# Optimization experiments

Hardware: AMD Instinct MI355X
Metric: run time of the kernel (lower is better)

Reference implementation:

```python
import jax, jax.numpy as jnp
import numpy as np

B, D, C = 512, 512, 100000
M1, M2, M3 = 1.0, 0.5, 0.0  # canonical ArcFace margins
EPS = 1e-12  # tf.nn.l2_normalize epsilon


def _l2norm(v, axis):
    return v * jax.lax.rsqrt(jnp.maximum(jnp.sum(v * v, axis=axis, keepdims=True), EPS))


def setup_inputs() -> dict:
    key = jax.random.key(0)
    k1, k2, k3 = jax.random.split(key, 3)
    x = jax.random.normal(k1, (B, D), dtype=jnp.float32)
    W = jax.random.normal(k2, (D, C), dtype=jnp.float32)
    label_idx = jax.random.randint(k3, (B,), 0, C, dtype=jnp.int32)
    return {"x": x, "W": W, "label_idx": label_idx}


def reference(x, W, label_idx):
    xn = _l2norm(x, axis=1)            # [B, D] unit embeddings
    Wn = _l2norm(W, axis=0)            # [D, C] unit class weights (norm=True fc)
    logits = xn @ Wn                   # [B, C] cosine similarities
    # gather target cosine per row (gather_nd over one-hot label)
    t = jnp.take_along_axis(logits, label_idx[:, None], axis=1)[:, 0]  # [B]
    # m1 == 1.0 -> skip angular scaling branch; m2 != 0 -> additive angular margin
    t = jnp.arccos(t) + M2
    # clamp to pi value-wise, straight-through gradient: t1 = t + pi - stop_grad(t)
    t = jnp.minimum(t, t + (jnp.pi - jax.lax.stop_gradient(t)))
    t = jnp.cos(t)
    onehot = jax.nn.one_hot(label_idx, C, dtype=logits.dtype)  # [B, C]
    out = logits * (1.0 - onehot) + t[:, None] * onehot
    out = out - onehot * M3
    return out
```

## Files before the change

### kernel.cpp

```cpp
#include <hip/hip_runtime.h>
#include <math.h>

#define BB 512
#define DD 512
#define CC 100000
#define MARGIN2 0.5f
#define PI_F 3.14159265358979323846f

#define BM 256
#define BN 128
#define BK 64
#define KSTEPS (DD / BK)
#define NPAN 782
#define GRID (2 * NPAN)

typedef __bf16 bf16x8 __attribute__((ext_vector_type(8)));
typedef float f32x4 __attribute__((ext_vector_type(4)));

static __device__ __forceinline__ unsigned short f2bf(float f) {
    union { float f; unsigned u; } v; v.f = f;
    unsigned r = v.u + 0x7FFFu + ((v.u >> 16) & 1u);
    return (unsigned short)(r >> 16);
}

static __device__ __forceinline__ int swz(int row, int kbyte) {
    return row * 128 + (kbyte ^ ((row & 7) << 4));
}

static __device__ __forceinline__ void gll16(const unsigned char* g, unsigned char* l) {
    __builtin_amdgcn_global_load_lds(
        (const __attribute__((address_space(1))) void*)g,
        (__attribute__((address_space(3))) void*)l, 16, 0, 0);
}

__global__ __launch_bounds__(256) void k_norm_x(const float* __restrict__ x,
                                                unsigned char* __restrict__ img) {
    const int lane = threadIdx.x & 63;
    const int row  = blockIdx.x * 4 + (threadIdx.x >> 6);
    const float* xr = x + (size_t)row * DD;
    float4 v0 = *(const float4*)(xr + lane * 4);
    float4 v1 = *(const float4*)(xr + lane * 4 + 256);
    float s = v0.x*v0.x + v0.y*v0.y + v0.z*v0.z + v0.w*v0.w
            + v1.x*v1.x + v1.y*v1.y + v1.z*v1.z + v1.w*v1.w;
    #pragma unroll
    for (int m = 32; m; m >>= 1) s += __shfl_xor(s, m, 64);
    float rs = rsqrtf(fmaxf(s, 1e-12f));
    ushort4 o0, o1;
    o0.x = f2bf(v0.x * rs); o0.y = f2bf(v0.y * rs);
    o0.z = f2bf(v0.z * rs); o0.w = f2bf(v0.w * rs);
    o1.x = f2bf(v1.x * rs); o1.y = f2bf(v1.y * rs);
    o1.z = f2bf(v1.z * rs); o1.w = f2bf(v1.w * rs);

    const int mb   = row >> 8;
    const int lrow = row & 255;
    const int k0   = lane * 4;
    const int t0   = k0 >> 6;
    const int c8   = (k0 >> 3) & 7;
    const int sub  = (k0 >> 2) & 1;
    const int base = (mb * 8 + t0) * 32768 + lrow * 128
                   + ((c8 * 16) ^ ((lrow & 7) << 4)) + sub * 8;
    *(ushort4*)(img + base)          = o0;
    *(ushort4*)(img + base + 131072) = o1;
}

#define LDSZ (65536 + 32768 + 512)

__global__ __launch_bounds__(512, 2) void k_gemm(const unsigned char* __restrict__ img,
                                                 const float* __restrict__ W,
                                                 float* __restrict__ out) {
    __shared__ __align__(16) unsigned char LDS[LDSZ];
    unsigned char* bufA = LDS;
    unsigned char* bufB = LDS + 65536;
    float* rn = (float*)(LDS + 98304);

    const int tid = threadIdx.x;
    const int bid = blockIdx.x;

    const int xcd = bid & 7;
    const int jj  = bid >> 3;
    const int v   = (xcd < 4) ? (xcd * 196 + jj) : (784 + (xcd - 4) * 195 + jj);
    const int mb  = v & 1;
    const int nb  = v >> 1;
    const int M0 = mb * BM;
    const int N0 = nb * BN;

    const int lane = tid & 63;
    const int wid  = tid >> 6;
    const int wm = wid >> 1;
    const int wn = wid & 1;
    const int lr = lane & 15;
    const int lg = lane >> 4;

    int b_go[4], b_ld[4];
    #pragma unroll
    for (int i = 0; i < 4; ++i) {
        int s  = tid + i * 512;
        int n  = s & 127;
        int kq = s >> 7;
        int col = N0 + n;
        col = col < CC ? col : CC - 1;
        b_go[i] = kq * 4 * CC + col;
        b_ld[i] = n * 128 + ((kq * 8) ^ ((n & 7) << 4));
    }

    const unsigned char* imgA = img + mb * (8 * 32768);
    const int lds_u = wid * 1024;

    float bregA[4][4], bregB[4][4];
    float bsq[4] = {0.f, 0.f, 0.f, 0.f};

#define LOAD_B(BREG, T) do {                                                   \
    _Pragma("unroll")                                                          \
    for (int i = 0; i < 4; ++i) {                                              \
        const float* p = W + b_go[i] + (T) * (BK * CC);                        \
        BREG[i][0] = p[0];      BREG[i][1] = p[CC];                            \
        BREG[i][2] = p[2 * CC]; BREG[i][3] = p[3 * CC];                        \
    } } while (0)

#define GLL_A(T) do {                                                          \
    unsigned char* A_nxt = bufA + ((T) & 1) * 32768;                           \
    const unsigned char* gsrc = imgA + (T) * 32768;                            \
    _Pragma("unroll")                                                          \
    for (int i = 0; i < 4; ++i)                                                \
        gll16(gsrc + i * 8192 + lds_u + lane * 16, A_nxt + i * 8192 + lds_u);  \
    } while (0)

#define WRITE_B(BREG, T) do {                                                  \
    unsigned char* dst = bufB + ((T) & 1) * 16384;                             \
    _Pragma("unroll")                                                          \
    for (int i = 0; i < 4; ++i) {                                              \
        bsq[i] += BREG[i][0] * BREG[i][0] + BREG[i][1] * BREG[i][1]            \
                + BREG[i][2] * BREG[i][2] + BREG[i][3] * BREG[i][3];           \
        unsigned w0, w1;                                                       \
        asm("v_cvt_pk_bf16_f32 %0, %1, %2" : "=v"(w0) : "v"(BREG[i][0]), "v"(BREG[i][1])); \
        asm("v_cvt_pk_bf16_f32 %0, %1, %2" : "=v"(w1) : "v"(BREG[i][2]), "v"(BREG[i][3])); \
        uint2 w; w.x = w0; w.y = w1;                                           \
        *(uint2*)(dst + b_ld[i]) = w;                                          \
    } } while (0)

#define COMPUTE(T) do {                                                        \
    const unsigned char* A_cur = bufA + ((T) & 1) * 32768;                     \
    const unsigned char* B_cur = bufB + ((T) & 1) * 16384;                     \
    _Pragma("unroll")                                                          \
    for (int ks = 0; ks < 2; ++ks) {                                           \
        bf16x8 af[4], bfr[4];                                                  \
        _Pragma("unroll")                                                      \
        for (int mf = 0; mf < 4; ++mf)                                         \
            af[mf] = *(const bf16x8*)(A_cur + swz(wm * 64 + mf * 16 + lr, ks * 64 + lg * 16)); \
        _Pragma("unroll")                                                      \
        for (int nf = 0; nf < 4; ++nf)                                         \
            bfr[nf] = *(const bf16x8*)(B_cur + swz(wn * 64 + nf * 16 + lr, ks * 64 + lg * 16)); \
        _Pragma("unroll")                                                      \
        for (int mf = 0; mf < 4; ++mf)                                         \
            _Pragma("unroll")                                                  \
            for (int nf = 0; nf < 4; ++nf)                                     \
                acc[mf][nf] = __builtin_amdgcn_mfma_f32_16x16x32_bf16(         \
                    bfr[nf], af[mf], acc[mf][nf], 0, 0, 0);                    \
    } } while (0)

#define KBODY(T, BC, BN_) do {                                                 \
    if ((T) + 1 < KSTEPS) GLL_A((T) + 1);            \
    if ((T) + 2 < KSTEPS) LOAD_B(BN_, (T) + 2);                                \
    __builtin_amdgcn_sched_barrier(0);                                         \
    COMPUTE(T);                                                                \
    if ((T) + 1 < KSTEPS) {                                                    \
        WRITE_B(BC, (T) + 1);                                                  \
        if ((T) + 2 < KSTEPS) { asm volatile("s_waitcnt vmcnt(16)" ::: "memory"); } \
        else                  { asm volatile("s_waitcnt vmcnt(0)"  ::: "memory"); } \
        __builtin_amdgcn_sched_barrier(0);                                     \
        asm volatile("s_waitcnt lgkmcnt(0)" ::: "memory");                     \
        __builtin_amdgcn_sched_barrier(0);                                     \
        __builtin_amdgcn_s_barrier();                                          \
        __builtin_amdgcn_sched_barrier(0);                                     \
    } } while (0)

    f32x4 acc[4][4];
    #pragma unroll
    for (int mf = 0; mf < 4; ++mf)
        #pragma unroll
        for (int nf = 0; nf < 4; ++nf)
            acc[mf][nf] = (f32x4)0.f;

    LOAD_B(bregA, 0);
    GLL_A(0);
    LOAD_B(bregB, 1);
    WRITE_B(bregA, 0);
    asm volatile("s_waitcnt vmcnt(16)" ::: "memory");
    __builtin_amdgcn_sched_barrier(0);
    asm volatile("s_waitcnt lgkmcnt(0)" ::: "memory");
    __builtin_amdgcn_sched_barrier(0);
    __builtin_amdgcn_s_barrier();
    __builtin_amdgcn_sched_barrier(0);

    KBODY(0, bregB, bregA);
    KBODY(1, bregA, bregB);
    KBODY(2, bregB, bregA);
    KBODY(3, bregA, bregB);
    KBODY(4, bregB, bregA);
    KBODY(5, bregA, bregB);
    KBODY(6, bregB, bregA);
    KBODY(7, bregA, bregB);

    __syncthreads();
    float* part = (float*)bufB;
    #pragma unroll
    for (int i = 0; i < 4; ++i)
        part[tid + i * 512] = bsq[i];
    __syncthreads();
    if (tid < BN) {
        float s = 0.f;
        #pragma unroll
        for (int k = 0; k < 16; ++k)
            s += part[k * BN + tid];
        rn[tid] = rsqrtf(fmaxf(s, 1e-12f));
    }
    __syncthreads();

    float* stag = (float*)bufA;
    #pragma unroll
    for (int rd = 0; rd < 8; ++rd) {
        if (wm == (rd >> 1)) {
            #pragma unroll
            for (int f = 0; f < 2; ++f) {
                const int mf = (rd & 1) * 2 + f;
                const int ml = f * 16 + lr;
                #pragma unroll
                for (int nf = 0; nf < 4; ++nf) {
                    const int nl = wn * 64 + nf * 16 + lg * 4;
                    const f32x4 rn4 = *(const f32x4*)(rn + nl);
                    f32x4 o;
                    #pragma unroll
                    for (int r = 0; r < 4; ++r)
                        o[r] = acc[mf][nf][r] * rn4[r];
                    *(f32x4*)(stag + ml * 132 + nl) = o;
                }
            }
        }
        __syncthreads();
        #pragma unroll
        for (int j = tid; j < 1024; j += 512) {
            const int m = j >> 5;
            const int n = (j & 31) * 4;
            if (N0 + n + 4 <= CC) {
                f32x4 o = *(const f32x4*)(stag + m * 132 + n);
                __builtin_nontemporal_store(o,
                    (f32x4*)(out + (size_t)(M0 + rd * 32 + m) * CC + N0 + n));
            }
        }
        __syncthreads();
    }
}

__global__ __launch_bounds__(512) void k_fix(const int* __restrict__ lab,
                                             float* __restrict__ out) {
    const int b = threadIdx.x;
    const int c = lab[b];
    const size_t idx = (size_t)b * CC + c;
    float t = out[idx];
    t = fminf(fmaxf(t, -1.f), 1.f);
    float th = acosf(t) + MARGIN2;
    th = fminf(th, PI_F);
    out[idx] = cosf(th);
}

extern "C" void kernel_launch(void* const* d_in, const int* in_sizes, int n_in,
                              void* d_out, int out_size, void* d_ws, size_t ws_size,
                              hipStream_t stream) {
    const float* x   = (const float*)d_in[0];
    const float* W   = (const float*)d_in[1];
    const int*   lab = (const int*)d_in[2];
    float* out = (float*)d_out;

    unsigned char* img = (unsigned char*)d_ws;

    k_norm_x<<<dim3(BB / 4), dim3(256), 0, stream>>>(x, img);
    k_gemm<<<dim3(GRID), dim3(512), 0, stream>>>(img, W, out);
    k_fix<<<dim3(1), dim3(512), 0, stream>>>(lab, out);
}
```

Baseline: 117.2 us.

## Load A fragments directly from global and shrink LDS for higher occupancy

The normalized x matrix is now written in plain row-major bf16, and each wave loads its MFMA A fragments straight from global memory into registers every k-step. This replaces the pre-swizzled image that was staged through LDS with global_load_lds. LDS use drops to just the double-buffered B tile, and launch bounds go from 2 to 4 blocks per CU so more waves can hide W load latency. The W prefetch is reorganized around a single register buffer: pack and write the next tile, then issue the following load. The trade-offs are unprefetched global A loads on the critical path, which rely on L2 hits, and a tighter VGPR budget that could cause spills.

```diff
diff --git a/kernel.cpp b/kernel.cpp
--- a/kernel.cpp
+++ b/kernel.cpp
@@ -27,14 +27,8 @@
     return row * 128 + (kbyte ^ ((row & 7) << 4));
 }
 
-static __device__ __forceinline__ void gll16(const unsigned char* g, unsigned char* l) {
-    __builtin_amdgcn_global_load_lds(
-        (const __attribute__((address_space(1))) void*)g,
-        (__attribute__((address_space(3))) void*)l, 16, 0, 0);
-}
-
 __global__ __launch_bounds__(256) void k_norm_x(const float* __restrict__ x,
-                                                unsigned char* __restrict__ img) {
+                                                unsigned short* __restrict__ xnb) {
     const int lane = threadIdx.x & 63;
     const int row  = blockIdx.x * 4 + (threadIdx.x >> 6);
     const float* xr = x + (size_t)row * DD;
@@ -50,28 +44,18 @@
     o0.z = f2bf(v0.z * rs); o0.w = f2bf(v0.w * rs);
     o1.x = f2bf(v1.x * rs); o1.y = f2bf(v1.y * rs);
     o1.z = f2bf(v1.z * rs); o1.w = f2bf(v1.w * rs);
-
-    const int mb   = row >> 8;
-    const int lrow = row & 255;
-    const int k0   = lane * 4;
-    const int t0   = k0 >> 6;
-    const int c8   = (k0 >> 3) & 7;
-    const int sub  = (k0 >> 2) & 1;
-    const int base = (mb * 8 + t0) * 32768 + lrow * 128
-                   + ((c8 * 16) ^ ((lrow & 7) << 4)) + sub * 8;
-    *(ushort4*)(img + base)          = o0;
-    *(ushort4*)(img + base + 131072) = o1;
-}
-
-#define LDSZ (65536 + 32768 + 512)
-
-__global__ __launch_bounds__(512, 2) void k_gemm(const unsigned char* __restrict__ img,
+    *(ushort4*)(xnb + (size_t)row * DD + lane * 4)       = o0;
+    *(ushort4*)(xnb + (size_t)row * DD + lane * 4 + 256) = o1;
+}
+
+#define LDSZ (32768 + 512)
+
+__global__ __launch_bounds__(512, 4) void k_gemm(const unsigned short* __restrict__ xnb,
                                                  const float* __restrict__ W,
                                                  float* __restrict__ out) {
     __shared__ __align__(16) unsigned char LDS[LDSZ];
-    unsigned char* bufA = LDS;
-    unsigned char* bufB = LDS + 65536;
-    float* rn = (float*)(LDS + 98304);
+    unsigned char* bufB = LDS;
+    float* rn = (float*)(LDS + 32768);
 
     const int tid = threadIdx.x;
     const int bid = blockIdx.x;
@@ -91,83 +75,82 @@
     const int lr = lane & 15;
     const int lg = lane >> 4;
 
-    int b_go[4], b_ld[4];
-    #pragma unroll
-    for (int i = 0; i < 4; ++i) {
-        int s  = tid + i * 512;
-        int n  = s & 127;
-        int kq = s >> 7;
-        int col = N0 + n;
-        col = col < CC ? col : CC - 1;
-        b_go[i] = kq * 4 * CC + col;
-        b_ld[i] = n * 128 + ((kq * 8) ^ ((n & 7) << 4));
-    }
-
-    const unsigned char* imgA = img + mb * (8 * 32768);
-    const int lds_u = wid * 1024;
-
-    float bregA[4][4], bregB[4][4];
-    float bsq[4] = {0.f, 0.f, 0.f, 0.f};
-
-#define LOAD_B(BREG, T) do {                                                   \
+    const unsigned short* aptr0 = xnb + (size_t)(M0 + wm * 64 +  0 + lr) * DD + lg * 8;
+    const unsigned short* aptr1 = xnb + (size_t)(M0 + wm * 64 + 16 + lr) * DD + lg * 8;
+    const unsigned short* aptr2 = xnb + (size_t)(M0 + wm * 64 + 32 + lr) * DD + lg * 8;
+    const unsigned short* aptr3 = xnb + (size_t)(M0 + wm * 64 + 48 + lr) * DD + lg * 8;
+
+    float    freg[4][4];
+    unsigned pk[8];
+    float    bsq[4] = {0.f, 0.f, 0.f, 0.f};
+    bf16x8   af[8];
+
+#define LOAD_B(T) do {                                                         \
     _Pragma("unroll")                                                          \
     for (int i = 0; i < 4; ++i) {                                              \
-        const float* p = W + b_go[i] + (T) * (BK * CC);                        \
-        BREG[i][0] = p[0];      BREG[i][1] = p[CC];                            \
-        BREG[i][2] = p[2 * CC]; BREG[i][3] = p[3 * CC];                        \
-    } } while (0)
-
-#define GLL_A(T) do {                                                          \
-    unsigned char* A_nxt = bufA + ((T) & 1) * 32768;                           \
-    const unsigned char* gsrc = imgA + (T) * 32768;                            \
-    _Pragma("unroll")                                                          \
-    for (int i = 0; i < 4; ++i)                                                \
-        gll16(gsrc + i * 8192 + lds_u + lane * 16, A_nxt + i * 8192 + lds_u);  \
+        const int s_ = tid + i * 512;                                          \
+        const int n_ = s_ & 127;                                               \
+        const int kq_ = s_ >> 7;                                               \
+        int col_ = N0 + n_; col_ = col_ < CC ? col_ : CC - 1;                  \
+        const float* p = W + (size_t)kq_ * 4 * CC + col_ + (size_t)(T) * (BK * CC); \
+        freg[i][0] = p[0];      freg[i][1] = p[CC];                            \
+        freg[i][2] = p[2 * CC]; freg[i][3] = p[3 * CC];                        \
+    } } while (0)
+
+#define PACK() do {                                                            \
+    _Pragma("unroll")                                                          \
+    for (int i = 0; i < 4; ++i) {                                              \
+        bsq[i] += freg[i][0] * freg[i][0] + freg[i][1] * freg[i][1]            \
+                + freg[i][2] * freg[i][2] + freg[i][3] * freg[i][3];           \
+        asm("v_cvt_pk_bf16_f32 %0, %1, %2" : "=v"(pk[2*i])   : "v"(freg[i][0]), "v"(freg[i][1])); \
+        asm("v_cvt_pk_bf16_f32 %0, %1, %2" : "=v"(pk[2*i+1]) : "v"(freg[i][2]), "v"(freg[i][3])); \
+    } } while (0)
+
+#define WRITE_PK(T) do {                                                       \
+    unsigned char* dst = bufB + ((T) & 1) * 16384;                             \
+    _Pragma("unroll")                                                          \
+    for (int i = 0; i < 4; ++i) {                                              \
+        const int s_ = tid + i * 512;                                          \
+        const int n_ = s_ & 127;                                               \
+        const int kq_ = s_ >> 7;                                               \
+        uint2 w; w.x = pk[2*i]; w.y = pk[2*i+1];                               \
+        *(uint2*)(dst + n_ * 128 + ((kq_ * 8) ^ ((n_ & 7) << 4))) = w;         \
+    } } while (0)
+
+#define LOAD_AF(T) do {                                                        \
+    af[0] = *(const bf16x8*)(aptr0 + (T) * 64);                                \
+    af[1] = *(const bf16x8*)(aptr1 + (T) * 64);                                \
+    af[2] = *(const bf16x8*)(aptr2 + (T) * 64);                                \
+    af[3] = *(const bf16x8*)(aptr3 + (T) * 64);                                \
+    af[4] = *(const bf16x8*)(aptr0 + (T) * 64 + 32);                           \
+    af[5] = *(const bf16x8*)(aptr1 + (T) * 64 + 32);                           \
+    af[6] = *(const bf16x8*)(aptr2 + (T) * 64 + 32);                           \
+    af[7] = *(const bf16x8*)(aptr3 + (T) * 64 + 32);                           \
     } while (0)
 
-#define WRITE_B(BREG, T) do {                                                  \
-    unsigned char* dst = bufB + ((T) & 1) * 16384;                             \
-    _Pragma("unroll")                                                          \
-    for (int i = 0; i < 4; ++i) {                                              \
-        bsq[i] += BREG[i][0] * BREG[i][0] + BREG[i][1] * BREG[i][1]            \
-                + BREG[i][2] * BREG[i][2] + BREG[i][3] * BREG[i][3];           \
-        unsigned w0, w1;                                                       \
-        asm("v_cvt_pk_bf16_f32 %0, %1, %2" : "=v"(w0) : "v"(BREG[i][0]), "v"(BREG[i][1])); \
-        asm("v_cvt_pk_bf16_f32 %0, %1, %2" : "=v"(w1) : "v"(BREG[i][2]), "v"(BREG[i][3])); \
-        uint2 w; w.x = w0; w.y = w1;                                           \
-        *(uint2*)(dst + b_ld[i]) = w;                                          \
-    } } while (0)
-
 #define COMPUTE(T) do {                                                        \
-    const unsigned char* A_cur = bufA + ((T) & 1) * 32768;                     \
     const unsigned char* B_cur = bufB + ((T) & 1) * 16384;                     \
     _Pragma("unroll")                                                          \
     for (int ks = 0; ks < 2; ++ks) {                                           \
-        bf16x8 af[4], bfr[4];                                                  \
         _Pragma("unroll")                                                      \
-        for (int mf = 0; mf < 4; ++mf)                                         \
-            af[mf] = *(const bf16x8*)(A_cur + swz(wm * 64 + mf * 16 + lr, ks * 64 + lg * 16)); \
-        _Pragma("unroll")                                                      \
-        for (int nf = 0; nf < 4; ++nf)                                         \
-            bfr[nf] = *(const bf16x8*)(B_cur + swz(wn * 64 + nf * 16 + lr, ks * 64 + lg * 16)); \
-        _Pragma("unroll")                                                      \
-        for (int mf = 0; mf < 4; ++mf)                                         \
+        for (int nf = 0; nf < 4; ++nf) {                                       \
+            bf16x8 bfr = *(const bf16x8*)(B_cur + swz(wn * 64 + nf * 16 + lr, ks * 64 + lg * 16)); \
             _Pragma("unroll")                                                  \
-            for (int nf = 0; nf < 4; ++nf)                                     \
+            for (int mf = 0; mf < 4; ++mf)                                     \
                 acc[mf][nf] = __builtin_amdgcn_mfma_f32_16x16x32_bf16(         \
-                    bfr[nf], af[mf], acc[mf][nf], 0, 0, 0);                    \
-    } } while (0)
-
-#define KBODY(T, BC, BN_) do {                                                 \
-    if ((T) + 1 < KSTEPS) GLL_A((T) + 1);            \
-    if ((T) + 2 < KSTEPS) LOAD_B(BN_, (T) + 2);                                \
+                    bfr, af[ks * 4 + mf], acc[mf][nf], 0, 0, 0);               \
+        }                                                                      \
+    } } while (0)
+
+#define KBODY(T) do {                                                          \
+    LOAD_AF(T);                                      \
+    __builtin_amdgcn_sched_barrier(0);                                         \
+    if ((T) + 1 < KSTEPS) { PACK(); WRITE_PK((T) + 1); }                       \
+    __builtin_amdgcn_sched_barrier(0);                                         \
+    if ((T) + 2 < KSTEPS) LOAD_B((T) + 2);       \
     __builtin_amdgcn_sched_barrier(0);                                         \
     COMPUTE(T);                                                                \
     if ((T) + 1 < KSTEPS) {                                                    \
-        WRITE_B(BC, (T) + 1);                                                  \
-        if ((T) + 2 < KSTEPS) { asm volatile("s_waitcnt vmcnt(16)" ::: "memory"); } \
-        else                  { asm volatile("s_waitcnt vmcnt(0)"  ::: "memory"); } \
-        __builtin_amdgcn_sched_barrier(0);                                     \
         asm volatile("s_waitcnt lgkmcnt(0)" ::: "memory");                     \
         __builtin_amdgcn_sched_barrier(0);                                     \
         __builtin_amdgcn_s_barrier();                                          \
@@ -181,25 +164,17 @@
         for (int nf = 0; nf < 4; ++nf)
             acc[mf][nf] = (f32x4)0.f;
 
-    LOAD_B(bregA, 0);
-    GLL_A(0);
-    LOAD_B(bregB, 1);
-    WRITE_B(bregA, 0);
-    asm volatile("s_waitcnt vmcnt(16)" ::: "memory");
-    __builtin_amdgcn_sched_barrier(0);
+    LOAD_B(0);
+    PACK();
+    WRITE_PK(0);
+    LOAD_B(1);
     asm volatile("s_waitcnt lgkmcnt(0)" ::: "memory");
     __builtin_amdgcn_sched_barrier(0);
     __builtin_amdgcn_s_barrier();
     __builtin_amdgcn_sched_barrier(0);
 
-    KBODY(0, bregB, bregA);
-    KBODY(1, bregA, bregB);
-    KBODY(2, bregB, bregA);
-    KBODY(3, bregA, bregB);
-    KBODY(4, bregB, bregA);
-    KBODY(5, bregA, bregB);
-    KBODY(6, bregB, bregA);
-    KBODY(7, bregA, bregB);
+    KBODY(0); KBODY(1); KBODY(2); KBODY(3);
+    KBODY(4); KBODY(5); KBODY(6); KBODY(7);
 
     __syncthreads();
     float* part = (float*)bufB;
@@ -216,7 +191,7 @@
     }
     __syncthreads();
 
-    float* stag = (float*)bufA;
+    float* stag = (float*)bufB;
     #pragma unroll
     for (int rd = 0; rd < 8; ++rd) {
         if (wm == (rd >> 1)) {
@@ -271,9 +246,9 @@
     const int*   lab = (const int*)d_in[2];
     float* out = (float*)d_out;
 
-    unsigned char* img = (unsigned char*)d_ws;
-
-    k_norm_x<<<dim3(BB / 4), dim3(256), 0, stream>>>(x, img);
-    k_gemm<<<dim3(GRID), dim3(512), 0, stream>>>(img, W, out);
+    unsigned short* xnb = (unsigned short*)d_ws;
+
+    k_norm_x<<<dim3(BB / 4), dim3(256), 0, stream>>>(x, xnb);
+    k_gemm<<<dim3(GRID), dim3(512), 0, stream>>>(xnb, W, out);
     k_fix<<<dim3(1), dim3(512), 0, stream>>>(lab, out);
 }
```

After: 211.3 us. 80.3% more time.
